# Kernel tuning notes

Measured on AMD Instinct MI355X. Metric: run time of the kernel, lower is better.

## Reference

```python
import jax, jax.numpy as jnp
import numpy as np

N_NODES = 50000
N_EDGES = 600000
D = 128
PROP_STEPS = 4


def setup_inputs() -> dict:
    key = jax.random.key(0)
    ks = jax.random.split(key, 9)
    d = D
    inp = {
        "nodes_ft": jax.random.normal(ks[0], (N_NODES, d), dtype=jnp.float32),
        "adj_list": jax.random.randint(ks[1], (2, N_EDGES), 0, N_NODES, dtype=jnp.int32),
        # nodes_adj_state_bias, xavier-normal style scale
        "bias": jax.random.normal(ks[2], (1, d), dtype=jnp.float32) * (2.0 / (1 + d)) ** 0.5,
        # gate Linears: weight [2d, d] (x @ W + b convention), xavier-ish scale
        "Wr": jax.random.normal(ks[3], (2 * d, d), dtype=jnp.float32) * (1.0 / (2 * d)) ** 0.5,
        "br": jnp.zeros((d,), dtype=jnp.float32),
        "Wz": jax.random.normal(ks[4], (2 * d, d), dtype=jnp.float32) * (1.0 / (2 * d)) ** 0.5,
        "bz": jnp.zeros((d,), dtype=jnp.float32),
        "Wt": jax.random.normal(ks[5], (2 * d, d), dtype=jnp.float32) * (1.0 / (2 * d)) ** 0.5,
        "bt": jnp.zeros((d,), dtype=jnp.float32),
    }
    return inp


def reference(nodes_ft, adj_list, bias, Wr, br, Wz, bz, Wt, bt):
    n = nodes_ft.shape[0]
    dst, src = adj_list[0], adj_list[1]
    prior_h = nodes_ft
    h = prior_h
    # Faithful to source: prior_h is NOT updated inside the loop (original code bug),
    # so each step recomputes the same h.
    for _ in range(PROP_STEPS):
        msg = prior_h[src]                                   # [E, d] gather
        agg = jax.ops.segment_sum(msg, dst, num_segments=n)  # [N, d] scatter-add
        s = jax.nn.softmax(agg + bias, axis=-1)              # [N, d]
        tmp = jnp.concatenate([s, prior_h], axis=-1)          # [N, 2d]
        r = jax.nn.sigmoid(tmp @ Wr + br)
        z = jax.nn.sigmoid(tmp @ Wz + bz)
        h_hat = jnp.tanh(jnp.concatenate([s, r * prior_h], axis=-1) @ Wt + bt)
        h = (1.0 - z) * prior_h + z * h_hat
    return h
```

## Files before the change

### kernel.cpp

```cpp
#include <hip/hip_runtime.h>

#define NN 50000
#define NE 600000
#define DD 128
#define CAP 64

typedef __attribute__((ext_vector_type(8))) short s16x8;
typedef __attribute__((ext_vector_type(4))) float f32x4;

#define CNT_BYTES   (256 * 1024)
#define SLOT_OFF    CNT_BYTES
#define SLOT_BYTES  ((size_t)NN * CAP * 2)
#define WPACK_OFF   (SLOT_OFF + SLOT_BYTES)
#define WPACK_N     (3 * 8 * 8 * 512)
#define WPACK_BYTES ((size_t)WPACK_N * 2)
#define NBF_OFF     (WPACK_OFF + WPACK_BYTES)

#define FILL_BLOCKS ((NE / 2 + 255) / 256)
#define CONV_BLOCKS (WPACK_N / 256)
#define NBF_BLOCKS  ((NN * DD / 8) / 256)

__device__ __forceinline__ unsigned short f2bf(float f) {
    unsigned int u = __float_as_uint(f);
    unsigned int r = (u + 0x7fffu + ((u >> 16) & 1u)) >> 16;
    return (unsigned short)r;
}
__device__ __forceinline__ float bf2f(unsigned short h) {
    return __uint_as_float(((unsigned int)h) << 16);
}
__device__ __forceinline__ void accum8(float* x, uint4 v, float msk) {
    x[0] = fmaf(__uint_as_float(v.x << 16),          msk, x[0]);
    x[1] = fmaf(__uint_as_float(v.x & 0xffff0000u),  msk, x[1]);
    x[2] = fmaf(__uint_as_float(v.y << 16),          msk, x[2]);
    x[3] = fmaf(__uint_as_float(v.y & 0xffff0000u),  msk, x[3]);
    x[4] = fmaf(__uint_as_float(v.z << 16),          msk, x[4]);
    x[5] = fmaf(__uint_as_float(v.z & 0xffff0000u),  msk, x[5]);
    x[6] = fmaf(__uint_as_float(v.w << 16),          msk, x[6]);
    x[7] = fmaf(__uint_as_float(v.w & 0xffff0000u),  msk, x[7]);
}

__global__ __launch_bounds__(256) void prep_k(
    const int* __restrict__ adj, int* __restrict__ cnt, unsigned short* __restrict__ slots,
    const float* __restrict__ Wr, const float* __restrict__ Wz,
    const float* __restrict__ Wt, unsigned short* __restrict__ wp,
    const float* __restrict__ nodes, unsigned short* __restrict__ nbf)
{
    int b = blockIdx.x;
    if (b < FILL_BLOCKS) {
        int t = b * 256 + threadIdx.x;
        if (2 * t >= NE) return;
        int2 d2 = *(const int2*)(adj + 2 * t);
        int2 s2 = *(const int2*)(adj + NE + 2 * t);
        int p0 = atomicAdd(&cnt[d2.x], 1);
        if (p0 < CAP) slots[(size_t)d2.x * CAP + p0] = (unsigned short)s2.x;
        int p1 = atomicAdd(&cnt[d2.y], 1);
        if (p1 < CAP) slots[(size_t)d2.y * CAP + p1] = (unsigned short)s2.y;
    } else if (b < FILL_BLOCKS + CONV_BLOCKS) {
        int t = (b - FILL_BLOCKS) * 256 + threadIdx.x;
        int j  = t & 7;
        int l  = (t >> 3) & 63;
        int kt = (t >> 9) & 7;
        int ct = (t >> 12) & 7;
        int g  = t >> 15;
        int k   = kt * 32 + ((l >> 4) & 3) * 8 + j;
        int col = ct * 16 + (l & 15);
        const float* W = (g == 0) ? Wr : (g == 1) ? Wz : Wt;
        wp[t] = f2bf(W[k * DD + col]);
    } else {
        int t = (b - FILL_BLOCKS - CONV_BLOCKS) * 256 + threadIdx.x;
        const float4* s4 = (const float4*)nodes + (size_t)t * 2;
        float4 a = s4[0], c4 = s4[1];
        uint4 o;
        o.x = (unsigned)f2bf(a.x)  | ((unsigned)f2bf(a.y)  << 16);
        o.y = (unsigned)f2bf(a.z)  | ((unsigned)f2bf(a.w)  << 16);
        o.z = (unsigned)f2bf(c4.x) | ((unsigned)f2bf(c4.y) << 16);
        o.w = (unsigned)f2bf(c4.z) | ((unsigned)f2bf(c4.w) << 16);
        ((uint4*)nbf)[t] = o;
    }
}

__global__ __launch_bounds__(256, 4) void fused_k(
    const unsigned short* __restrict__ nbf,
    const int* __restrict__ adj,
    const int* __restrict__ cnt,
    const unsigned short* __restrict__ slots,
    const unsigned short* __restrict__ wp,
    const float* __restrict__ bias,
    const float* __restrict__ br, const float* __restrict__ bz, const float* __restrict__ bt,
    float* __restrict__ out)
{
    __shared__ unsigned short X[64][264];
    const int tid  = threadIdx.x;
    const int w    = tid >> 6;
    const int l    = tid & 63;
    const int row0 = blockIdx.x * 64;
    const int q    = l >> 4;
    const int li   = l & 15;

    {
        const float4 bb0 = *(const float4*)(bias + 8 * li);
        const float4 bb1 = *(const float4*)(bias + 8 * li + 4);
        int rown  = row0 + (w << 4) + li;
        int c_all = cnt[rown < NN ? rown : 0];

        unsigned short sraw[2];
        uint4 vg[2][4]; float mg[2][4];
        uint4 phg[2];
        int   slotm[2], cj[2];

        {
            int g0 = row0 + (w << 4);
            int gc0 = g0 < NN ? g0 : 0;
            int gc1 = (g0 + 1) < NN ? (g0 + 1) : 0;
            sraw[0] = slots[(size_t)gc0 * CAP + l];
            sraw[1] = slots[(size_t)gc1 * CAP + l];
            cj[0] = __shfl(c_all, 0);
            slotm[0] = (l < cj[0]) ? (int)sraw[0] : 0;
            if (q == 1) phg[0] = *(const uint4*)(nbf + (size_t)gc0 * DD + 8 * li);
#pragma unroll
            for (int i = 0; i < 4; ++i) {
                int sp = i * 4 + q;
                int s0 = __shfl(slotm[0], sp);
                vg[0][i] = *(const uint4*)(nbf + (size_t)s0 * DD + 8 * li);
                mg[0][i] = (sp < cj[0]) ? 1.f : 0.f;
            }
        }

#pragma unroll
        for (int j = 0; j < 16; ++j) {
            const int p = j & 1, pn = p ^ 1;
            unsigned short snew = 0;
            if (j + 2 < 16) {
                int g2 = row0 + (w << 4) + j + 2;
                int gc2 = g2 < NN ? g2 : 0;
                snew = slots[(size_t)gc2 * CAP + l];
            }
            if (j + 1 < 16) {
                int g1 = row0 + (w << 4) + j + 1;
                int gc1 = g1 < NN ? g1 : 0;
                cj[pn] = __shfl(c_all, j + 1);
                slotm[pn] = (l < cj[pn]) ? (int)sraw[pn] : 0;
                if (q == 1) phg[pn] = *(const uint4*)(nbf + (size_t)gc1 * DD + 8 * li);
#pragma unroll
                for (int i = 0; i < 4; ++i) {
                    int sp = i * 4 + q;
                    int s0 = __shfl(slotm[pn], sp);
                    vg[pn][i] = *(const uint4*)(nbf + (size_t)s0 * DD + 8 * li);
                    mg[pn][i] = (sp < cj[pn]) ? 1.f : 0.f;
                }
            }
            int lr   = (w << 4) + j;
            int grow = row0 + lr;
            int c    = cj[p];
            float x[8];
#pragma unroll
            for (int i = 0; i < 8; ++i) x[i] = 0.f;
            if (c <= CAP) {
#pragma unroll
                for (int i = 0; i < 4; ++i) accum8(x, vg[p][i], mg[p][i]);
                for (int jj = 16; jj < c; jj += 16) {
                    uint4 v[4]; float msk[4];
#pragma unroll
                    for (int i = 0; i < 4; ++i) {
                        int sp = jj + i * 4 + q;
                        int s0 = __shfl(slotm[p], sp & 63);
                        v[i] = *(const uint4*)(nbf + (size_t)s0 * DD + 8 * li);
                        msk[i] = (sp < c) ? 1.f : 0.f;
                    }
#pragma unroll
                    for (int i = 0; i < 4; ++i) accum8(x, v[i], msk[i]);
                }
            } else {
                int mi = 0;
                for (int base = 0; base < NE; base += 64) {
                    int e  = base + l;
                    int d  = (e < NE) ? adj[e] : -1;
                    int sv = (e < NE) ? adj[NE + e] : 0;
                    unsigned long long m = __ballot(d == grow);
                    while (m) {
                        int bpos = __ffsll((unsigned long long)m) - 1;
                        m &= m - 1;
                        int s0 = __shfl(sv, bpos);
                        if ((mi & 3) == q) {
                            uint4 v = *(const uint4*)(nbf + (size_t)s0 * DD + 8 * li);
                            accum8(x, v, 1.f);
                        }
                        ++mi;
                    }
                }
            }
#pragma unroll
            for (int i = 0; i < 8; ++i) {
                x[i] += __shfl_xor(x[i], 16);
                x[i] += __shfl_xor(x[i], 32);
            }
            x[0] += bb0.x; x[1] += bb0.y; x[2] += bb0.z; x[3] += bb0.w;
            x[4] += bb1.x; x[5] += bb1.y; x[6] += bb1.z; x[7] += bb1.w;
            float mx = x[0];
#pragma unroll
            for (int i = 1; i < 8; ++i) mx = fmaxf(mx, x[i]);
#pragma unroll
            for (int o = 1; o < 16; o <<= 1) mx = fmaxf(mx, __shfl_xor(mx, o));
            float e8[8], sm = 0.f;
#pragma unroll
            for (int i = 0; i < 8; ++i) { e8[i] = __expf(x[i] - mx); sm += e8[i]; }
#pragma unroll
            for (int o = 1; o < 16; o <<= 1) sm += __shfl_xor(sm, o);
            float inv = 1.f / sm;
            if (q == 0) {
                uint4 u;
                u.x = (unsigned)f2bf(e8[0] * inv) | ((unsigned)f2bf(e8[1] * inv) << 16);
                u.y = (unsigned)f2bf(e8[2] * inv) | ((unsigned)f2bf(e8[3] * inv) << 16);
                u.z = (unsigned)f2bf(e8[4] * inv) | ((unsigned)f2bf(e8[5] * inv) << 16);
                u.w = (unsigned)f2bf(e8[6] * inv) | ((unsigned)f2bf(e8[7] * inv) << 16);
                *(uint4*)&X[lr][8 * li] = u;
            } else if (q == 1) {
                *(uint4*)&X[lr][128 + 8 * li] = phg[p];
            }
            sraw[p] = snew;
        }
    }

    const int rbase  = w * 16;
    const int mrow   = l & 15;
    const int quad   = l >> 4;
    const int col_in = l & 15;
    const int rq     = l >> 4;

    s16x8 a[8];
#pragma unroll
    for (int kt = 0; kt < 8; ++kt)
        a[kt] = *(const s16x8*)&X[rbase + mrow][kt * 32 + quad * 8];

    const s16x8* wp8 = (const s16x8*)wp;
    float zv[8][4];

#pragma unroll
    for (int ct = 0; ct < 8; ++ct) {
        int c = ct * 16 + col_in;
        float brv = br[c], bzv = bz[c];
        f32x4 ar = {brv, brv, brv, brv};
        f32x4 az = {bzv, bzv, bzv, bzv};
#pragma unroll
        for (int kt = 0; kt < 8; ++kt) {
            s16x8 bfr = wp8[((0 * 8 + ct) * 8 + kt) * 64 + l];
            s16x8 bfz = wp8[((1 * 8 + ct) * 8 + kt) * 64 + l];
            ar = __builtin_amdgcn_mfma_f32_16x16x32_bf16(a[kt], bfr, ar, 0, 0, 0);
            az = __builtin_amdgcn_mfma_f32_16x16x32_bf16(a[kt], bfz, az, 0, 0, 0);
        }
#pragma unroll
        for (int i = 0; i < 4; ++i) {
            float rr = 1.f / (1.f + __expf(-ar[i]));
            zv[ct][i] = 1.f / (1.f + __expf(-az[i]));
            int lr = rbase + rq * 4 + i;
            float ph = bf2f(X[lr][128 + c]);
            X[lr][c] = f2bf(rr * ph);
        }
    }

#pragma unroll
    for (int kt = 4; kt < 8; ++kt)
        a[kt] = *(const s16x8*)&X[rbase + mrow][(kt - 4) * 32 + quad * 8];

#pragma unroll
    for (int ct = 0; ct < 8; ++ct) {
        int c = ct * 16 + col_in;
        float btv = bt[c];
        f32x4 at = {btv, btv, btv, btv};
#pragma unroll
        for (int kt = 0; kt < 8; ++kt) {
            s16x8 bft = wp8[((2 * 8 + ct) * 8 + kt) * 64 + l];
            at = __builtin_amdgcn_mfma_f32_16x16x32_bf16(a[kt], bft, at, 0, 0, 0);
        }
#pragma unroll
        for (int i = 0; i < 4; ++i) {
            int lr   = rbase + rq * 4 + i;
            int grow = row0 + lr;
            if (grow < NN) {
                float hh = tanhf(at[i]);
                float z  = zv[ct][i];
                float ph = bf2f(X[lr][128 + c]);
                out[(size_t)grow * DD + c] = (1.f - z) * ph + z * hh;
            }
        }
    }
}

extern "C" void kernel_launch(void* const* d_in, const int* in_sizes, int n_in,
                              void* d_out, int out_size, void* d_ws, size_t ws_size,
                              hipStream_t stream) {
    const float* nodes = (const float*)d_in[0];
    const int*   adj   = (const int*)d_in[1];
    const float* bias  = (const float*)d_in[2];
    const float* Wr    = (const float*)d_in[3];
    const float* br    = (const float*)d_in[4];
    const float* Wz    = (const float*)d_in[5];
    const float* bz    = (const float*)d_in[6];
    const float* Wt    = (const float*)d_in[7];
    const float* bt    = (const float*)d_in[8];
    float* out = (float*)d_out;

    char* ws = (char*)d_ws;
    int*            cnt   = (int*)ws;
    unsigned short* slots = (unsigned short*)(ws + SLOT_OFF);
    unsigned short* wpack = (unsigned short*)(ws + WPACK_OFF);
    unsigned short* nbf   = (unsigned short*)(ws + NBF_OFF);

    hipMemsetAsync(cnt, 0, (size_t)NN * sizeof(int), stream);

    prep_k<<<FILL_BLOCKS + CONV_BLOCKS + NBF_BLOCKS, 256, 0, stream>>>(
        adj, cnt, slots, Wr, Wz, Wt, wpack, nodes, nbf);
    fused_k<<<(NN + 63) / 64, 256, 0, stream>>>(nbf, adj, cnt, slots, wpack,
                                                bias, br, bz, bt, out);
}
```

Measured before the change: 205.2 us.

## Merge prep and fused kernels into one launch with a grid-wide barrier

Folds the edge-bucketing, weight packing and bf16 node conversion into the start of the main kernel. Each block handles a grid-strided share of that work, then all blocks wait on a global atomic spin barrier before the aggregation/GRU phase. This removes one kernel launch and its inter-kernel gap. It relies on all 782 blocks being co-resident (256 threads, 4 blocks/CU bound); if they are not, the barrier deadlocks. The memset now also zeroes the barrier counter.

```diff
diff --git a/kernel.cpp b/kernel.cpp
--- a/kernel.cpp
+++ b/kernel.cpp
@@ -4,21 +4,19 @@
 #define NE 600000
 #define DD 128
 #define CAP 64
+#define GRID ((NN + 63) / 64)
 
 typedef __attribute__((ext_vector_type(8))) short s16x8;
 typedef __attribute__((ext_vector_type(4))) float f32x4;
 
 #define CNT_BYTES   (256 * 1024)
+#define BAR_OFF     200064
 #define SLOT_OFF    CNT_BYTES
 #define SLOT_BYTES  ((size_t)NN * CAP * 2)
 #define WPACK_OFF   (SLOT_OFF + SLOT_BYTES)
 #define WPACK_N     (3 * 8 * 8 * 512)
 #define WPACK_BYTES ((size_t)WPACK_N * 2)
 #define NBF_OFF     (WPACK_OFF + WPACK_BYTES)
-
-#define FILL_BLOCKS ((NE / 2 + 255) / 256)
-#define CONV_BLOCKS (WPACK_N / 256)
-#define NBF_BLOCKS  ((NN * DD / 8) / 256)
 
 __device__ __forceinline__ unsigned short f2bf(float f) {
     unsigned int u = __float_as_uint(f);
@@ -39,56 +37,73 @@
     x[7] = fmaf(__uint_as_float(v.w & 0xffff0000u),  msk, x[7]);
 }
 
-__global__ __launch_bounds__(256) void prep_k(
-    const int* __restrict__ adj, int* __restrict__ cnt, unsigned short* __restrict__ slots,
+__global__ __launch_bounds__(256, 4) void mega_k(
+    const float* __restrict__ nodes,
+    const int* __restrict__ adj,
+    int* __restrict__ cnt,
+    unsigned int* __restrict__ barrier,
+    unsigned short* __restrict__ slots,
+    unsigned short* __restrict__ wp,
+    unsigned short* __restrict__ nbf,
+    const float* __restrict__ bias,
     const float* __restrict__ Wr, const float* __restrict__ Wz,
-    const float* __restrict__ Wt, unsigned short* __restrict__ wp,
-    const float* __restrict__ nodes, unsigned short* __restrict__ nbf)
-{
-    int b = blockIdx.x;
-    if (b < FILL_BLOCKS) {
-        int t = b * 256 + threadIdx.x;
-        if (2 * t >= NE) return;
-        int2 d2 = *(const int2*)(adj + 2 * t);
-        int2 s2 = *(const int2*)(adj + NE + 2 * t);
-        int p0 = atomicAdd(&cnt[d2.x], 1);
-        if (p0 < CAP) slots[(size_t)d2.x * CAP + p0] = (unsigned short)s2.x;
-        int p1 = atomicAdd(&cnt[d2.y], 1);
-        if (p1 < CAP) slots[(size_t)d2.y * CAP + p1] = (unsigned short)s2.y;
-    } else if (b < FILL_BLOCKS + CONV_BLOCKS) {
-        int t = (b - FILL_BLOCKS) * 256 + threadIdx.x;
-        int j  = t & 7;
-        int l  = (t >> 3) & 63;
-        int kt = (t >> 9) & 7;
-        int ct = (t >> 12) & 7;
-        int g  = t >> 15;
-        int k   = kt * 32 + ((l >> 4) & 3) * 8 + j;
-        int col = ct * 16 + (l & 15);
-        const float* W = (g == 0) ? Wr : (g == 1) ? Wz : Wt;
-        wp[t] = f2bf(W[k * DD + col]);
-    } else {
-        int t = (b - FILL_BLOCKS - CONV_BLOCKS) * 256 + threadIdx.x;
-        const float4* s4 = (const float4*)nodes + (size_t)t * 2;
-        float4 a = s4[0], c4 = s4[1];
-        uint4 o;
-        o.x = (unsigned)f2bf(a.x)  | ((unsigned)f2bf(a.y)  << 16);
-        o.y = (unsigned)f2bf(a.z)  | ((unsigned)f2bf(a.w)  << 16);
-        o.z = (unsigned)f2bf(c4.x) | ((unsigned)f2bf(c4.y) << 16);
-        o.w = (unsigned)f2bf(c4.z) | ((unsigned)f2bf(c4.w) << 16);
-        ((uint4*)nbf)[t] = o;
-    }
-}
-
-__global__ __launch_bounds__(256, 4) void fused_k(
-    const unsigned short* __restrict__ nbf,
-    const int* __restrict__ adj,
-    const int* __restrict__ cnt,
-    const unsigned short* __restrict__ slots,
-    const unsigned short* __restrict__ wp,
-    const float* __restrict__ bias,
-    const float* __restrict__ br, const float* __restrict__ bz, const float* __restrict__ bt,
+    const float* __restrict__ Wt,
+    const float* __restrict__ br, const float* __restrict__ bz,
+    const float* __restrict__ bt,
     float* __restrict__ out)
 {
+    {
+        const int gtid = blockIdx.x * 256 + threadIdx.x;
+        const int nthr = GRID * 256;
+#pragma unroll
+        for (int i = 0; i < 3; ++i) {
+            int e = gtid + i * nthr;
+            if (e < NE) {
+                int d = adj[e];
+                int s = adj[NE + e];
+                int pos = atomicAdd(&cnt[d], 1);
+                if (pos < CAP) slots[(size_t)d * CAP + pos] = (unsigned short)s;
+            }
+        }
+        if (gtid < WPACK_N) {
+            int t = gtid;
+            int j  = t & 7;
+            int l  = (t >> 3) & 63;
+            int kt = (t >> 9) & 7;
+            int ct = (t >> 12) & 7;
+            int g  = t >> 15;
+            int k   = kt * 32 + ((l >> 4) & 3) * 8 + j;
+            int col = ct * 16 + (l & 15);
+            const float* W = (g == 0) ? Wr : (g == 1) ? Wz : Wt;
+            wp[t] = f2bf(W[k * DD + col]);
+        }
+#pragma unroll
+        for (int i = 0; i < 4; ++i) {
+            int t = gtid + i * nthr;
+            if (t < NN * DD / 8) {
+                const float4* s4 = (const float4*)nodes + (size_t)t * 2;
+                float4 a = s4[0], c4 = s4[1];
+                uint4 o;
+                o.x = (unsigned)f2bf(a.x)  | ((unsigned)f2bf(a.y)  << 16);
+                o.y = (unsigned)f2bf(a.z)  | ((unsigned)f2bf(a.w)  << 16);
+                o.z = (unsigned)f2bf(c4.x) | ((unsigned)f2bf(c4.y) << 16);
+                o.w = (unsigned)f2bf(c4.z) | ((unsigned)f2bf(c4.w) << 16);
+                ((uint4*)nbf)[t] = o;
+            }
+        }
+    }
+    __threadfence();
+    __syncthreads();
+    if (threadIdx.x == 0) {
+        __hip_atomic_fetch_add(barrier, 1u, __ATOMIC_ACQ_REL, __HIP_MEMORY_SCOPE_AGENT);
+        while (__hip_atomic_load(barrier, __ATOMIC_ACQUIRE, __HIP_MEMORY_SCOPE_AGENT)
+               < (unsigned)GRID) {
+            __builtin_amdgcn_s_sleep(8);
+        }
+    }
+    __syncthreads();
+    __threadfence();
+
     __shared__ unsigned short X[64][264];
     const int tid  = threadIdx.x;
     const int w    = tid >> 6;
@@ -302,14 +317,13 @@
 
     char* ws = (char*)d_ws;
     int*            cnt   = (int*)ws;
+    unsigned int*   bar   = (unsigned int*)(ws + BAR_OFF);
     unsigned short* slots = (unsigned short*)(ws + SLOT_OFF);
     unsigned short* wpack = (unsigned short*)(ws + WPACK_OFF);
     unsigned short* nbf   = (unsigned short*)(ws + NBF_OFF);
 
-    hipMemsetAsync(cnt, 0, (size_t)NN * sizeof(int), stream);
-
-    prep_k<<<FILL_BLOCKS + CONV_BLOCKS + NBF_BLOCKS, 256, 0, stream>>>(
-        adj, cnt, slots, Wr, Wz, Wt, wpack, nodes, nbf);
-    fused_k<<<(NN + 63) / 64, 256, 0, stream>>>(nbf, adj, cnt, slots, wpack,
-                                                bias, br, bz, bt, out);
-}
+    hipMemsetAsync(ws, 0, CNT_BYTES, stream);
+
+    mega_k<<<GRID, 256, 0, stream>>>(nodes, adj, cnt, bar, slots, wpack, nbf,
+                                     bias, Wr, Wz, Wt, br, bz, bt, out);
+}
```

New measurement: 443.2 us. 2.16x slower.
